# Optimization experiments

Hardware: AMD Instinct MI355X
Metric: run time of the kernel (lower is better)

Reference implementation:

```python
import jax, jax.numpy as jnp
import numpy as np
from jax import lax

B, C, H, W = 2, 64, 96, 192
D = 48          # max_disp
G = 8           # num_groups
GC = C // G     # group channels
OUT = 32        # out_channels


def conv2d(x, w, pad):
    return lax.conv_general_dilated(x, w, (1, 1), [(pad, pad)] * 2,
                                    dimension_numbers=('NCHW', 'OIHW', 'NCHW'))


def conv3d(x, w, dil, pad):
    return lax.conv_general_dilated(x, w, (1, 1, 1), [(pad, pad)] * 3,
                                    rhs_dilation=(dil, dil, dil),
                                    dimension_numbers=('NCDHW', 'OIDHW', 'NCDHW'))


def setup_inputs() -> dict:
    key = jax.random.key(0)
    ks = jax.random.split(key, 9)
    s = 0.05
    return dict(
        feat_l=jax.random.normal(ks[0], (B, C, H, W), jnp.float32),
        feat_r=jax.random.normal(ks[1], (B, C, H, W), jnp.float32),
        edge_mask=jax.random.uniform(ks[2], (B, 1, H, W), jnp.float32),
        w_pred1=jax.random.normal(ks[3], (32, C + 1, 3, 3), jnp.float32) * s,
        bn_gamma=jnp.ones((32,), jnp.float32),
        bn_beta=jnp.zeros((32,), jnp.float32),
        bn_mean=jnp.zeros((32,), jnp.float32),
        bn_var=jnp.ones((32,), jnp.float32),
        w_pred2=jax.random.normal(ks[4], (3, 32, 1, 1), jnp.float32) * s,
        b_pred2=jnp.zeros((3,), jnp.float32),
        temp=jnp.ones((1,), jnp.float32),
        w_s=jax.random.normal(ks[5], (G, G, 3, 3, 3), jnp.float32) * s,
        w_m=jax.random.normal(ks[6], (G, G, 3, 3, 3), jnp.float32) * s,
        w_l=jax.random.normal(ks[7], (G, G, 3, 3, 3), jnp.float32) * s,
        w_final=jax.random.normal(ks[8], (OUT, G, 1, 1, 1), jnp.float32) * s,
        b_final=jnp.zeros((OUT,), jnp.float32),
    )


def _forward(feat_l, feat_r, edge_mask, w_pred1, bn_gamma, bn_beta, bn_mean,
             bn_var, w_pred2, b_pred2, temp, w_s, w_m, w_l, w_final, b_final):
    # --- group-wise normalized correlation volume ---
    fl = feat_l.reshape(B, G, GC, H, W)
    fr = feat_r.reshape(B, G, GC, H, W)
    eps = 1e-12
    fl = fl / jnp.maximum(jnp.linalg.norm(fl, axis=2, keepdims=True), eps)
    fr = fr / jnp.maximum(jnp.linalg.norm(fr, axis=2, keepdims=True), eps)
    pad = D - 1
    fr_pad = jnp.pad(fr, ((0, 0), (0, 0), (0, 0), (0, 0), (pad, 0)))
    inv = np.float32(1.0 / np.sqrt(GC))

    def body(_, d):
        shifted = lax.dynamic_slice_in_dim(fr_pad, pad - d, W, axis=4)
        corr = jnp.sum(fl * shifted, axis=2) * inv  # [B,G,H,W]
        return None, corr

    _, vols = lax.scan(body, None, jnp.arange(D))          # [D,B,G,H,W]
    base = jnp.transpose(vols, (1, 2, 0, 3, 4))            # [B,G,D,H,W]

    # --- scale predictor (conv -> BN(eval) -> relu -> 1x1 conv) ---
    x = jnp.concatenate([feat_l, edge_mask], axis=1)       # [B,C+1,H,W]
    x = conv2d(x, w_pred1, 1)
    x = (x - bn_mean[:, None, None]) * (bn_gamma[:, None, None]
         / jnp.sqrt(bn_var[:, None, None] + 1e-5)) + bn_beta[:, None, None]
    x = jax.nn.relu(x)
    logits = conv2d(x, w_pred2, 0) + b_pred2[:, None, None]  # [B,3,H,W]
    t = jnp.maximum(temp, 0.1)
    sw = jax.nn.softmax(logits / t, axis=1)
    w_s_exp = sw[:, 0:1, None]   # [B,1,1,H,W]
    w_m_exp = sw[:, 1:2, None]
    w_l_exp = sw[:, 2:3, None]

    # --- multi-dilation 3D aggregation fused by predicted weights ---
    fused = (conv3d(base, w_s, 1, 1) * w_s_exp
             + conv3d(base, w_m, 2, 2) * w_m_exp
             + conv3d(base, w_l, 4, 4) * w_l_exp)
    out = conv3d(fused, w_final, 1, 0) + b_final[None, :, None, None, None]
    return out


def reference(feat_l, feat_r, edge_mask, w_pred1, bn_gamma, bn_beta, bn_mean,
              bn_var, w_pred2, b_pred2, temp, w_s, w_m, w_l, w_final, b_final):
    return _forward(feat_l, feat_r, edge_mask, w_pred1, bn_gamma, bn_beta,
                    bn_mean, bn_var, w_pred2, b_pred2, temp, w_s, w_m, w_l,
                    w_final, b_final)
```

## Files before the change

### kernel.cpp

```cpp
#include <hip/hip_runtime.h>
#include <hip/hip_bf16.h>

#define B_   2
#define C_   64
#define H_   96
#define W_   192
#define D_   48
#define G_   8
#define OUT_ 32
#define HW_  (H_ * W_)

#define DP_ 56
#define HP_ 104
#define WP_ 200
#define PLANE_ (HP_ * WP_ * 8)
#define BASEH_HALFS (B_ * DP_ * PLANE_)

#define OFF_BASEH 4718592
#define OFF_SW    14036992
#define OFF_BPACK 14147584
#define OFF_WP1T  14158336

typedef _Float16 f16x8  __attribute__((ext_vector_type(8)));
typedef float    f32x4  __attribute__((ext_vector_type(4)));
typedef float    f32x16 __attribute__((ext_vector_type(16)));

__global__ void wtrans_kernel(const float* __restrict__ w_s,
                              const float* __restrict__ w_m,
                              const float* __restrict__ w_l,
                              const float* __restrict__ w_final,
                              const float* __restrict__ w_pred1,
                              _Float16* __restrict__ bpack,
                              float* __restrict__ wp1T) {
    int i = blockIdx.x * 256 + threadIdx.x;
    if (i < 21504) {
        int j = i & 7;
        int lane = (i >> 3) & 63;
        int kc = i >> 9;
        int c = kc % 14, k = kc / 14;
        int hf = lane >> 5, n = lane & 31;
        int kd = 0, kh = 0, kw = 0; bool valid = true;
        if (c < 9)        { kd = hf ? 1 : -1; kh = c / 3 - 1; kw = c % 3 - 1; }
        else if (c < 12)  { kd = 0; kh = hf ? 1 : -1; kw = (c - 9) - 1; }
        else if (c == 12) { kd = 0; kh = 0; kw = hf ? 1 : -1; }
        else              { valid = (hf == 0); }
        float val = 0.f;
        if (valid) {
            int tap = (kd + 1) * 9 + (kh + 1) * 3 + (kw + 1);
            const float* wsel = (k == 0) ? w_s : (k == 1) ? w_m : w_l;
            #pragma unroll
            for (int g = 0; g < 8; ++g)
                val += w_final[n * 8 + g] * wsel[(g * 8 + j) * 27 + tap];
        }
        bpack[i] = (_Float16)val;
    } else if (i < 21504 + 18720) {
        int j = i - 21504;
        int oc = j & 31; int it = j >> 5; int ic = it / 9; int t = it - ic * 9;
        wp1T[j] = w_pred1[(oc * 65 + ic) * 9 + t];
    }
}

__global__ __launch_bounds__(256) void corr_kernel(const float* __restrict__ feat_l,
                                                   const float* __restrict__ feat_r,
                                                   _Float16* __restrict__ baseh) {
    __shared__ float frl[80 * 68];
    int tid = threadIdx.x;
    int h = blockIdx.y;
    int b = blockIdx.z;
    int w0 = blockIdx.x * 32;
    int wbase = w0 - 48;

    for (int p = tid; p < 640; p += 256) {
        int gg = p / 80;
        int iw = p - gg * 80;
        int wg = wbase + iw;
        if (wg >= 0) {
            const float* src = feat_r + (size_t)(b * 64 + gg * 8) * HW_ + h * W_ + wg;
            float v[8]; float s = 0.f;
            #pragma unroll
            for (int c = 0; c < 8; ++c) { v[c] = src[(size_t)c * HW_]; s += v[c] * v[c]; }
            float inv = 0.35355339059327373f / fmaxf(sqrtf(s), 1e-12f);
            #pragma unroll
            for (int c = 0; c < 8; ++c) frl[iw * 68 + gg * 8 + c] = v[c] * inv;
        }
    }

    int g = tid & 7, wi = tid >> 3;
    int w = w0 + wi;
    const float* fls = feat_l + (size_t)(b * 64 + g * 8) * HW_ + h * W_ + w;
    float a[8]; float s = 0.f;
    #pragma unroll
    for (int c = 0; c < 8; ++c) { a[c] = fls[(size_t)c * HW_]; s += a[c] * a[c]; }
    float inv = 1.0f / fmaxf(sqrtf(s), 1e-12f);
    #pragma unroll
    for (int c = 0; c < 8; ++c) a[c] *= inv;

    __syncthreads();

    _Float16* dst = baseh + (size_t)((b * DP_ + 4) * HP_ + 4 + h) * WP_ * 8 + (size_t)(4 + w) * 8 + g;
    for (int d = 0; d < D_; ++d) {
        int wd = w - d;
        float acc = 0.f;
        if (wd >= 0) {
            const float* fr = frl + (wd - wbase) * 68 + g * 8;
            acc = a[0]*fr[0] + a[1]*fr[1] + a[2]*fr[2] + a[3]*fr[3]
                + a[4]*fr[4] + a[5]*fr[5] + a[6]*fr[6] + a[7]*fr[7];
        }
        dst[(size_t)d * PLANE_] = (_Float16)acc;
    }
}

__global__ __launch_bounds__(256) void pred_kernel(const float* __restrict__ feat_l,
                                                   const float* __restrict__ edge,
                                                   const float* __restrict__ wp1T,
                                                   const float* __restrict__ gamma,
                                                   const float* __restrict__ beta,
                                                   const float* __restrict__ mean,
                                                   const float* __restrict__ var,
                                                   const float* __restrict__ w2,
                                                   const float* __restrict__ b2,
                                                   const float* __restrict__ temp,
                                                   float* __restrict__ swp) {
    int pid = blockIdx.x * 256 + threadIdx.x;
    int b = pid / HW_; int hw = pid - b * HW_;
    int h = hw / W_;   int w = hw - h * W_;

    float acc[32];
    #pragma unroll
    for (int i = 0; i < 32; ++i) acc[i] = 0.f;

    for (int ic = 0; ic < 65; ++ic) {
        const float* src = (ic < 64) ? (feat_l + (size_t)(b * 64 + ic) * HW_)
                                     : (edge + (size_t)b * HW_);
        float v[9];
        #pragma unroll
        for (int ky = 0; ky < 3; ++ky) {
            int y = h + ky - 1;
            #pragma unroll
            for (int kx = 0; kx < 3; ++kx) {
                int x = w + kx - 1;
                bool ok = (y >= 0) && (y < H_) && (x >= 0) && (x < W_);
                v[ky * 3 + kx] = ok ? src[y * W_ + x] : 0.f;
            }
        }
        #pragma unroll
        for (int t = 0; t < 9; ++t) {
            const float* wrow = wp1T + (ic * 9 + t) * 32;
            float vv = v[t];
            #pragma unroll
            for (int oc = 0; oc < 32; ++oc) acc[oc] = fmaf(vv, wrow[oc], acc[oc]);
        }
    }

    float l0 = b2[0], l1 = b2[1], l2 = b2[2];
    #pragma unroll
    for (int oc = 0; oc < 32; ++oc) {
        float sc = gamma[oc] / sqrtf(var[oc] + 1e-5f);
        float xb = (acc[oc] - mean[oc]) * sc + beta[oc];
        float r = fmaxf(xb, 0.f);
        l0 = fmaf(w2[0 * 32 + oc], r, l0);
        l1 = fmaf(w2[1 * 32 + oc], r, l1);
        l2 = fmaf(w2[2 * 32 + oc], r, l2);
    }
    float t = fmaxf(temp[0], 0.1f);
    float it = 1.0f / t;
    l0 *= it; l1 *= it; l2 *= it;
    float m = fmaxf(l0, fmaxf(l1, l2));
    float e0 = __expf(l0 - m), e1 = __expf(l1 - m), e2 = __expf(l2 - m);
    float is = 1.0f / (e0 + e1 + e2);
    swp[0 * (B_ * HW_) + pid] = e0 * is;
    swp[1 * (B_ * HW_) + pid] = e1 * is;
    swp[2 * (B_ * HW_) + pid] = e2 * is;
}

__global__ __launch_bounds__(256, 2) void fusedconv_mfma32(
        const _Float16* __restrict__ baseh,
        const float* __restrict__ swp,
        const _Float16* __restrict__ bpack,
        const float* __restrict__ bf,
        float* __restrict__ out) {
    __shared__ _Float16 bsh[3 * 14 * 64 * 8];

    int tid = threadIdx.x;
    {
        const f16x8* srcv = (const f16x8*)bpack;
        f16x8* dstv = (f16x8*)bsh;
        for (int i = tid; i < 2688; i += 256) dstv[i] = srcv[i];
    }

    int L   = blockIdx.x + 6 * (blockIdx.y + 48 * blockIdx.z);
    int sL  = (L & 7) * 288 + (L >> 3);
    int bx  = sL % 6;
    int byz = sL / 6;
    int by  = byz % 48;
    int bz  = byz / 48;

    int wave = tid >> 6, lane = tid & 63;
    int m = lane & 31, hf = lane >> 5;
    int hh = wave >> 1, dh = wave & 1;
    int w0 = bx * 32;
    int h  = by * 2 + hh;
    int b  = bz >> 2;
    int dq = bz & 3;
    int d0 = dq * 12 + dh * 6;

    f16x8 swh[3];
    #pragma unroll
    for (int k = 0; k < 3; ++k) {
        float s = swp[k * (B_ * HW_) + b * HW_ + h * W_ + w0 + m];
        _Float16 hs = (_Float16)s;
        f16x8 t;
        #pragma unroll
        for (int j = 0; j < 8; ++j) t[j] = hs;
        swh[k] = t;
    }

    int hdv[3][4];
    #pragma unroll
    for (int k = 0; k < 3; ++k) {
        int dil = 1 << k;
        hdv[k][0] = hf * (2 * dil * HP_ * WP_ * 8 * 2);
        hdv[k][1] = hf * (2 * dil * WP_ * 8 * 2);
        hdv[k][2] = hf * (2 * dil * 8 * 2);
        hdv[k][3] = 0;
    }

    const char* bb = (const char*)baseh;
    char*       ob = (char*)out;

    unsigned pm = (unsigned)(((((b * DP_ + 4 + d0) * HP_ + 4 + h) * WP_ + 4 + w0 + m) * 8) * 2);
    float bias = bf[m];
    unsigned outoff = (unsigned)((((b * OUT_ + m) * D_ + d0) * HW_ + h * W_ + w0 + 4 * hf) * 4);

    __syncthreads();

    for (int d = 0; d < 6; ++d) {
        unsigned bofs = (unsigned)(lane * 16);
        asm volatile("" : "+v"(bofs));
        const char* bshp = (const char*)bsh + bofs;

        f32x16 acc0, acc1;
        #pragma unroll
        for (int i = 0; i < 16; ++i) { acc0[i] = 0.f; acc1[i] = 0.f; }
        #pragma unroll
        for (int k = 0; k < 3; ++k) {
            int dil = 1 << k;
            #pragma unroll
            for (int c = 0; c < 14; ++c) {
                int coff, cls;
                if (c < 9)        { coff = ((-dil * HP_ + (c / 3 - 1) * dil) * WP_ * 8 + (c % 3 - 1) * dil * 8) * 2; cls = 0; }
                else if (c < 12)  { coff = ((-dil) * WP_ * 8 + ((c - 9) - 1) * dil * 8) * 2;                          cls = 1; }
                else if (c == 12) { coff = -dil * 16;                                                                  cls = 2; }
                else              { coff = 0;                                                                          cls = 3; }
                unsigned a = pm + (unsigned)(hdv[k][cls] + coff);
                f16x8 av = *(const f16x8*)(bb + a);
                f16x8 Bv = *(const f16x8*)(bshp + (k * 14 + c) * 1024);
                av = av * swh[k];
                if (c & 1) acc1 = __builtin_amdgcn_mfma_f32_32x32x16_f16(av, Bv, acc1, 0, 0, 0);
                else       acc0 = __builtin_amdgcn_mfma_f32_32x32x16_f16(av, Bv, acc0, 0, 0, 0);
            }
        }
        #pragma unroll
        for (int q = 0; q < 4; ++q) {
            f32x4 v;
            #pragma unroll
            for (int i = 0; i < 4; ++i) v[i] = acc0[4 * q + i] + acc1[4 * q + i] + bias;
            *(f32x4*)(ob + outoff + q * 32) = v;
        }
        pm += PLANE_ * 2;
        outoff += HW_ * 4;
    }
}

extern "C" void kernel_launch(void* const* d_in, const int* in_sizes, int n_in,
                              void* d_out, int out_size, void* d_ws, size_t ws_size,
                              hipStream_t stream) {
    const float* feat_l   = (const float*)d_in[0];
    const float* feat_r   = (const float*)d_in[1];
    const float* edge     = (const float*)d_in[2];
    const float* w_pred1  = (const float*)d_in[3];
    const float* bn_gamma = (const float*)d_in[4];
    const float* bn_beta  = (const float*)d_in[5];
    const float* bn_mean  = (const float*)d_in[6];
    const float* bn_var   = (const float*)d_in[7];
    const float* w_pred2  = (const float*)d_in[8];
    const float* b_pred2  = (const float*)d_in[9];
    const float* temp     = (const float*)d_in[10];
    const float* w_s      = (const float*)d_in[11];
    const float* w_m      = (const float*)d_in[12];
    const float* w_l      = (const float*)d_in[13];
    const float* w_final  = (const float*)d_in[14];
    const float* b_final  = (const float*)d_in[15];
    float* out = (float*)d_out;

    float* ws = (float*)d_ws;
    _Float16*  baseh = (_Float16*)(ws + OFF_BASEH);
    float*     swp   = ws + OFF_SW;
    _Float16*  bpack = (_Float16*)(ws + OFF_BPACK);
    float*     wp1T  = ws + OFF_WP1T;

    wtrans_kernel<<<dim3(158), 256, 0, stream>>>(w_s, w_m, w_l, w_final, w_pred1, bpack, wp1T);
    hipMemsetAsync(baseh, 0, (size_t)BASEH_HALFS * sizeof(_Float16), stream);
    corr_kernel<<<dim3(W_ / 32, H_, B_), 256, 0, stream>>>(feat_l, feat_r, baseh);
    pred_kernel<<<dim3(B_ * HW_ / 256), 256, 0, stream>>>(feat_l, edge, wp1T, bn_gamma,
                                                          bn_beta, bn_mean, bn_var,
                                                          w_pred2, b_pred2, temp, swp);
    fusedconv_mfma32<<<dim3(W_ / 32, H_ / 2, B_ * 4), 256, 0, stream>>>(baseh, swp, bpack, b_final, out);
}
```

Before: 482.9 us.

## Replace full-buffer memset with halo-only zeroing and batch MFMA operand loads

The full memset of the padded fp16 cost volume is removed. Extra blocks in the correlation kernel now zero only the padding halo (the outer depth planes plus the H/W border rows and columns), so the interior is written once by the correlation blocks. The fused conv kernel also issues all 42 A-operand loads up front, then scales and runs the MFMAs at raised wave priority to overlap memory latency. This costs many more registers for the 42 f16x8 values, which may lower occupancy. Correctness depends on the interior being fully written by the correlation blocks.

```diff
diff --git a/kernel.cpp b/kernel.cpp
--- a/kernel.cpp
+++ b/kernel.cpp
@@ -65,6 +65,35 @@
                                                    _Float16* __restrict__ baseh) {
     __shared__ float frl[80 * 68];
     int tid = threadIdx.x;
+
+    if (blockIdx.y >= 96) {
+        int e = (int)(blockIdx.y - 96) * 12 + (int)blockIdx.x * 2 + (int)blockIdx.z;
+        if (e < 112) {
+            int b  = e / 56;
+            int dp = e - b * 56;
+            f16x8* pl = (f16x8*)(baseh + (size_t)(b * DP_ + dp) * PLANE_);
+            f16x8 z;
+            #pragma unroll
+            for (int j = 0; j < 8; ++j) z[j] = (_Float16)0.f;
+            if (dp < 4 || dp >= 52) {
+                for (int i = tid; i < 20800; i += 256) pl[i] = z;
+            } else {
+                for (int i = tid; i < 1600; i += 256) {
+                    int r = i / 200, cc = i - (i / 200) * 200;
+                    int hp = (r < 4) ? r : 96 + r;
+                    pl[hp * 200 + cc] = z;
+                }
+                for (int i = tid; i < 768; i += 256) {
+                    int r = i >> 3, cc = i & 7;
+                    int hp = 4 + r;
+                    int wp = (cc < 4) ? cc : 192 + cc;
+                    pl[hp * 200 + wp] = z;
+                }
+            }
+        }
+        return;
+    }
+
     int h = blockIdx.y;
     int b = blockIdx.z;
     int w0 = blockIdx.x * 32;
@@ -239,9 +268,7 @@
         asm volatile("" : "+v"(bofs));
         const char* bshp = (const char*)bsh + bofs;
 
-        f32x16 acc0, acc1;
-        #pragma unroll
-        for (int i = 0; i < 16; ++i) { acc0[i] = 0.f; acc1[i] = 0.f; }
+        f16x8 av[42];
         #pragma unroll
         for (int k = 0; k < 3; ++k) {
             int dil = 1 << k;
@@ -253,13 +280,29 @@
                 else if (c == 12) { coff = -dil * 16;                                                                  cls = 2; }
                 else              { coff = 0;                                                                          cls = 3; }
                 unsigned a = pm + (unsigned)(hdv[k][cls] + coff);
-                f16x8 av = *(const f16x8*)(bb + a);
+                av[k * 14 + c] = *(const f16x8*)(bb + a);
+            }
+        }
+        __builtin_amdgcn_s_setprio(1);
+        #pragma unroll
+        for (int k = 0; k < 3; ++k)
+            #pragma unroll
+            for (int c = 0; c < 14; ++c)
+                av[k * 14 + c] = av[k * 14 + c] * swh[k];
+        f32x16 acc0, acc1;
+        #pragma unroll
+        for (int i = 0; i < 16; ++i) { acc0[i] = 0.f; acc1[i] = 0.f; }
+        #pragma unroll
+        for (int k = 0; k < 3; ++k) {
+            #pragma unroll
+            for (int c = 0; c < 14; ++c) {
                 f16x8 Bv = *(const f16x8*)(bshp + (k * 14 + c) * 1024);
-                av = av * swh[k];
-                if (c & 1) acc1 = __builtin_amdgcn_mfma_f32_32x32x16_f16(av, Bv, acc1, 0, 0, 0);
-                else       acc0 = __builtin_amdgcn_mfma_f32_32x32x16_f16(av, Bv, acc0, 0, 0, 0);
+                if (c & 1) acc1 = __builtin_amdgcn_mfma_f32_32x32x16_f16(av[k * 14 + c], Bv, acc1, 0, 0, 0);
+                else       acc0 = __builtin_amdgcn_mfma_f32_32x32x16_f16(av[k * 14 + c], Bv, acc0, 0, 0, 0);
             }
         }
+        __builtin_amdgcn_s_setprio(0);
+
         #pragma unroll
         for (int q = 0; q < 4; ++q) {
             f32x4 v;
@@ -300,8 +343,7 @@
     float*     wp1T  = ws + OFF_WP1T;
 
     wtrans_kernel<<<dim3(158), 256, 0, stream>>>(w_s, w_m, w_l, w_final, w_pred1, bpack, wp1T);
-    hipMemsetAsync(baseh, 0, (size_t)BASEH_HALFS * sizeof(_Float16), stream);
-    corr_kernel<<<dim3(W_ / 32, H_, B_), 256, 0, stream>>>(feat_l, feat_r, baseh);
+    corr_kernel<<<dim3(W_ / 32, 106, B_), 256, 0, stream>>>(feat_l, feat_r, baseh);
     pred_kernel<<<dim3(B_ * HW_ / 256), 256, 0, stream>>>(feat_l, edge, wp1T, bn_gamma,
                                                           bn_beta, bn_mean, bn_var,
                                                           w_pred2, b_pred2, temp, swp);
```

Measured after the change: 483.1 us. Within noise of the previous version (+0.0%).
